# Kernel tuning notes

Measured on AMD Instinct MI355X. Metric: run time of the kernel, lower is better.

Reference implementation:

```python
import jax, jax.numpy as jnp
import numpy as np

CODEBOOK_SIZE = 1024
EMB_DIM = 256
BETA = 0.25


def setup_inputs() -> dict:
    key = jax.random.key(0)
    k1, k2 = jax.random.split(key)
    z = jax.random.normal(k1, (8, EMB_DIM, 16, 16, 16), dtype=jnp.float32)
    # torch init: uniform(-1/K, 1/K)
    emb = jax.random.uniform(k2, (CODEBOOK_SIZE, EMB_DIM), dtype=jnp.float32,
                             minval=-1.0 / CODEBOOK_SIZE, maxval=1.0 / CODEBOOK_SIZE)
    return {"z": z, "emb": emb}


def reference(z, emb):
    b, c, h, w, dd = z.shape
    K = emb.shape[0]
    # (b c h w d) -> (b h w d, c)
    zf = jnp.transpose(z, (0, 2, 3, 4, 1)).reshape(-1, c)  # [N, C]
    d = ((zf ** 2).sum(axis=1, keepdims=True)
         + (emb ** 2).sum(axis=1)
         - 2.0 * zf @ emb.T)  # [N, K]
    mean_distance = jnp.mean(d)
    idx = jnp.argmin(d, axis=1)  # [N]
    # one-hot @ codebook == gather
    zq = jnp.take(emb, idx, axis=0)  # [N, C]
    zq = jnp.transpose(zq.reshape(b, h, w, dd, c), (0, 4, 1, 2, 3))  # [b,c,h,w,d]
    loss = (jnp.mean((jax.lax.stop_gradient(zq) - z) ** 2)
            + BETA * jnp.mean((zq - jax.lax.stop_gradient(z)) ** 2))
    # straight-through estimator
    zq_st = z + jax.lax.stop_gradient(zq - z)
    # perplexity from code usage histogram (== mean of one-hot encodings)
    counts = jnp.zeros((K,), dtype=z.dtype).at[idx].add(1.0)
    e_mean = counts / idx.shape[0]
    perplexity = jnp.exp(-jnp.sum(e_mean * jnp.log(e_mean + 1e-10)))
    return zq_st, loss, perplexity, idx, mean_distance
```

## Files before the change

kernel.cpp:

```cpp
#include <hip/hip_runtime.h>
#include <math.h>

#define C 256
#define K 1024
#define SS 4096
#define NB 8
#define NN 32768
#define ZQ_ELEMS 8388608
#define OUT_LOSS 8388608
#define OUT_PERP 8388609
#define OUT_IDX  8388610
#define OUT_MD   8421378

#define WS_SZ2   0
#define WS_SE2   1
#define WS_LOSS  2
#define WS_ZSUM  8
#define WS_ESUM  264
#define WS_CNT   520
#define WS_E2R   1544
#define WS_Z2N   2568
#define WS_FLG   35336
#define WS_EH    68608
#define WS_CAND  330752

#define TC_FACT 1.8e-6f
#define TF_FACT 1.6e-6f
#define CAP 4
#define CAP_BIG 24
#define OV 7

typedef __attribute__((ext_vector_type(8))) short short8;
typedef __attribute__((ext_vector_type(4))) float f32x4;
typedef unsigned short u16;

__device__ inline u16 f2bf(float x) {
  unsigned u = __float_as_uint(x);
  unsigned r = (u + 0x7fffu + ((u >> 16) & 1u)) >> 16;
  return (u16)r;
}
__device__ inline float bf2f(u16 h) { return __uint_as_float(((unsigned)h) << 16); }

__device__ __forceinline__ void gl_lds16(const u16* g, u16* l) {
  __builtin_amdgcn_global_load_lds(
      (const __attribute__((address_space(1))) unsigned int*)g,
      (__attribute__((address_space(3))) unsigned int*)l,
      16, 0, 0);
}

__device__ inline float np_sumsq_256(const float* __restrict__ a) {
  float tot = 0.f;
  #pragma unroll
  for (int h = 0; h < 2; ++h) {
    const float* p = a + 128 * h;
    float r[8];
    #pragma unroll
    for (int j = 0; j < 8; ++j) r[j] = __fmul_rn(p[j], p[j]);
    for (int i = 8; i < 128; i += 8) {
      #pragma unroll
      for (int j = 0; j < 8; ++j) {
        float v = p[i + j];
        r[j] = __fadd_rn(r[j], __fmul_rn(v, v));
      }
    }
    float s01 = __fadd_rn(r[0], r[1]);
    float s23 = __fadd_rn(r[2], r[3]);
    float s45 = __fadd_rn(r[4], r[5]);
    float s67 = __fadd_rn(r[6], r[7]);
    float res = __fadd_rn(__fadd_rn(s01, s23), __fadd_rn(s45, s67));
    tot = (h == 0) ? res : __fadd_rn(tot, res);
  }
  return tot;
}

__global__ __launch_bounds__(256)
void emb_prep_k(const float* __restrict__ emb, float* __restrict__ ws,
                u16* __restrict__ eh) {
  int r0 = blockIdx.x * 16;
  int t = threadIdx.x;
  float s = 0.f;
  #pragma unroll
  for (int i = 0; i < 16; ++i) {
    size_t idx = (size_t)(r0 + i) * C + t;
    float v = emb[idx];
    s += v;
    eh[idx] = f2bf(v);
  }
  atomicAdd(&ws[WS_ESUM + t], s);
  if (t < 16) {
    float e2 = np_sumsq_256(emb + (size_t)(r0 + t) * C);
    ws[WS_E2R + r0 + t] = e2;
    atomicAdd(&ws[WS_SE2], e2);
  }
}

#define MROWS 64
#define ZS_STRIDE 260

__global__ __launch_bounds__(256)
void prep_z_k(const float* __restrict__ z, float* __restrict__ ws,
              u16* __restrict__ zh_g) {
  __shared__ float zs[MROWS * ZS_STRIDE];
  const int t = threadIdx.x;
  const int n0 = blockIdx.x * MROWS;
  const int b = n0 / SS;
  const int s0 = n0 % SS;
  {
    const int sl = t & 63, cg = t >> 6;
    const float* zb = z + (size_t)b * C * SS + s0 + sl;
    #pragma unroll
    for (int i = 0; i < 16; ++i) {
      int c = (cg * 16 + i) * 4;
      float4 v;
      v.x = zb[(size_t)(c + 0) * SS];
      v.y = zb[(size_t)(c + 1) * SS];
      v.z = zb[(size_t)(c + 2) * SS];
      v.w = zb[(size_t)(c + 3) * SS];
      *(float4*)&zs[sl * ZS_STRIDE + c] = v;
    }
  }
  __syncthreads();
  {
    float s = 0.f;
    #pragma unroll 8
    for (int r = 0; r < MROWS; ++r) s += zs[r * ZS_STRIDE + t];
    atomicAdd(&ws[WS_ZSUM + t], s);
  }
  {
    #pragma unroll
    for (int i = 0; i < 8; ++i) {
      int q = i * 256 + t;
      int row = q >> 5;
      int c0 = (q & 31) * 8;
      float4 va = *(const float4*)&zs[row * ZS_STRIDE + c0];
      float4 vb = *(const float4*)&zs[row * ZS_STRIDE + c0 + 4];
      float f[8] = {va.x, va.y, va.z, va.w, vb.x, vb.y, vb.z, vb.w};
      short8 hv;
      #pragma unroll
      for (int j = 0; j < 8; ++j) hv[j] = (short)f2bf(f[j]);
      *(short8*)&zh_g[(size_t)(n0 + row) * C + c0] = hv;
    }
  }
  if (t < MROWS) {
    float z2 = np_sumsq_256(&zs[t * ZS_STRIDE]);
    ws[WS_Z2N + n0 + t] = z2;
    #pragma unroll
    for (int off = 32; off; off >>= 1) z2 += __shfl_down(z2, off);
    if (t == 0) atomicAdd(&ws[WS_SZ2], z2);
  }
}

#define BM 64
#define BN 128
#define CH 64

__global__ __launch_bounds__(256, 2)
void vq_mfma_k(const u16* __restrict__ zh_g, const u16* __restrict__ eh_g,
               const float* __restrict__ e2row, const float* __restrict__ z2np,
               float* __restrict__ out_idx,
               int* __restrict__ qarr, u16* __restrict__ cand) {
  extern __shared__ u16 smem_u16[];
  u16* Ah2 = smem_u16;
  u16* Bh2 = Ah2 + 2 * BM * CH;
  float* e2s = (float*)(Bh2 + 2 * BN * CH);
  float* z2s = e2s + BN;
  float* lval = z2s + BM;
  unsigned* Mlds = (unsigned*)(lval + BM * CAP_BIG);
  unsigned* cntl = Mlds + BM;
  u16* lidx = (u16*)(cntl + BM);

  const int t = threadIdx.x;
  const int lane = t & 63;
  const int wid = t >> 6;
  const int wm = wid >> 1, wn = wid & 1;
  const int quad = lane >> 4, lr = lane & 15;
  const int row0 = blockIdx.x * BM;
  const int wrow = lane >> 3;
  const int pl = wrow * C + ((lane & 7) ^ wrow) * 8;

  if (t < BM) {
    z2s[t] = z2np[row0 + t];
    Mlds[t] = 0x7F800000u;
    cntl[t] = 0u;
  }

  {
    #pragma unroll
    for (int i = 0; i < 2; ++i) {
      int grow = (wid * 2 + i) * 8;
      gl_lds16(&zh_g[(size_t)(row0 + grow) * C + pl], &Ah2[grow * CH]);
    }
    #pragma unroll
    for (int i = 0; i < 4; ++i) {
      int grow = (wid * 4 + i) * 8;
      gl_lds16(&eh_g[(size_t)grow * C + pl], &Bh2[grow * CH]);
    }
  }
  __syncthreads();

  float v1[8], i1f[8];
  #pragma unroll
  for (int s = 0; s < 8; ++s) { v1[s] = 3.4e38f; i1f[s] = 0.f; }

  f32x4 acc[2][4];
  #pragma unroll
  for (int mi = 0; mi < 2; ++mi)
    #pragma unroll
    for (int ni = 0; ni < 4; ++ni) acc[mi][ni] = (f32x4){0.f, 0.f, 0.f, 0.f};

  int p = 0;
  for (int it = 0; it < 32; ++it) {
    const int nt = it >> 2, ch = it & 3;
    if (ch == 0 && t < BN) e2s[t] = e2row[nt * BN + t];
    if (it < 31) {
      const int ntn = (it + 1) >> 2, chn = (it + 1) & 3;
      const int c0n = chn * CH;
      u16* Ab = Ah2 + (p ^ 1) * (BM * CH);
      u16* Bb = Bh2 + (p ^ 1) * (BN * CH);
      #pragma unroll
      for (int i = 0; i < 2; ++i) {
        int grow = (wid * 2 + i) * 8;
        gl_lds16(&zh_g[(size_t)(row0 + grow) * C + c0n + pl], &Ab[grow * CH]);
      }
      #pragma unroll
      for (int i = 0; i < 4; ++i) {
        int grow = (wid * 4 + i) * 8;
        gl_lds16(&eh_g[(size_t)(ntn * BN + grow) * C + c0n + pl], &Bb[grow * CH]);
      }
    }
    {
      const u16* Ab = Ah2 + p * (BM * CH);
      const u16* Bb = Bh2 + p * (BN * CH);
      #pragma unroll
      for (int s = 0; s < 2; ++s) {
        const int q = s * 4 + quad;
        short8 af[2];
        #pragma unroll
        for (int mi = 0; mi < 2; ++mi) {
          int rowl = wm * 32 + mi * 16 + lr;
          int jp = q ^ (rowl & 7);
          af[mi] = *(const short8*)&Ab[rowl * CH + jp * 8];
        }
        #pragma unroll
        for (int ni = 0; ni < 4; ++ni) {
          int rowb = wn * 64 + ni * 16 + lr;
          int jp = q ^ (rowb & 7);
          short8 bh = *(const short8*)&Bb[rowb * CH + jp * 8];
          #pragma unroll
          for (int mi = 0; mi < 2; ++mi)
            acc[mi][ni] = __builtin_amdgcn_mfma_f32_16x16x32_bf16(af[mi], bh, acc[mi][ni], 0, 0, 0);
        }
      }
    }
    if (ch == 3) {
      const int kc0 = nt * BN;
      #pragma unroll
      for (int mi = 0; mi < 2; ++mi)
        #pragma unroll
        for (int r = 0; r < 4; ++r) {
          const int slot = mi * 4 + r;
          const int row = wm * 32 + mi * 16 + quad * 4 + r;
          const float z2r = z2s[row];
          float dqv[4];
          #pragma unroll
          for (int ni = 0; ni < 4; ++ni)
            dqv[ni] = __fsub_rn(__fadd_rn(z2r, e2s[wn * 64 + ni * 16 + lr]),
                                __fmul_rn(2.f, acc[mi][ni][r]));
          float mm = fminf(fminf(dqv[0], dqv[1]), fminf(dqv[2], dqv[3]));
          #pragma unroll
          for (int off = 1; off < 16; off <<= 1)
            mm = fminf(mm, __shfl_xor(mm, off));
          if (lr == 0) atomicMin(&Mlds[row], __float_as_uint(mm));
          float Mst = __uint_as_float(Mlds[row]);
          float base = fminf(mm, Mst);
          float thr = fmaf(base, TC_FACT, base);
          #pragma unroll
          for (int ni = 0; ni < 4; ++ni) {
            float dq = dqv[ni];
            int col = kc0 + wn * 64 + ni * 16 + lr;
            if (dq < v1[slot]) { v1[slot] = dq; i1f[slot] = (float)col; }
            if (dq < thr) {
              unsigned pp = atomicAdd(&cntl[row], 1u);
              if (pp < CAP_BIG) {
                lval[row * CAP_BIG + pp] = dq;
                lidx[row * CAP_BIG + pp] = (u16)col;
              }
            }
            acc[mi][ni][r] = 0.f;
          }
        }
    }
    __syncthreads();
    p ^= 1;
  }

  #pragma unroll
  for (int off = 1; off < 16; off <<= 1) {
    #pragma unroll
    for (int s = 0; s < 8; ++s) {
      float ov1 = __shfl_xor(v1[s], off);
      float oi1 = __shfl_xor(i1f[s], off);
      bool take = (ov1 < v1[s]) || (ov1 == v1[s] && oi1 < i1f[s]);
      if (take) { v1[s] = ov1; i1f[s] = oi1; }
    }
  }
  __syncthreads();
  float* mv1 = (float*)Ah2;
  float* mi1 = mv1 + 2 * BM;
  if (lr == 0) {
    #pragma unroll
    for (int mi = 0; mi < 2; ++mi)
      #pragma unroll
      for (int r = 0; r < 4; ++r) {
        int slot = mi * 4 + r;
        int row = wm * 32 + mi * 16 + quad * 4 + r;
        mv1[wn * BM + row] = v1[slot];
        mi1[wn * BM + row] = i1f[slot];
      }
  }
  __syncthreads();
  if (t < BM) {
    float a1 = mv1[t], ai = mi1[t];
    float c1 = mv1[BM + t], ci = mi1[BM + t];
    bool take = (c1 < a1) || (c1 == a1 && ci < ai);
    float b1 = take ? c1 : a1;
    float bi = take ? ci : ai;
    out_idx[row0 + t] = bi;
    unsigned raw = cntl[t];
    float tf = fmaf(b1, TF_FACT, b1);
    int c = 0;
    u16 keep[CAP];
    bool ovf = raw > (unsigned)CAP_BIG;
    if (!ovf) {
      for (unsigned j = 0; j < raw; ++j) {
        if (lval[t * CAP_BIG + j] <= tf) {
          if (c < CAP) keep[c] = lidx[t * CAP_BIG + j];
          ++c;
        }
      }
      if (c > CAP) ovf = true;
    }
    if (ovf) {
      int o = atomicAdd(&qarr[1], 1);
      qarr[2 + NN - 1 - o] = row0 + t;
    } else if (c > 1) {
      int q = atomicAdd(&qarr[0], 1);
      qarr[2 + q] = (row0 + t) | (c << 16);
      #pragma unroll
      for (int j = 0; j < CAP; ++j)
        cand[(size_t)q * CAP + j] = (j < c) ? keep[j] : (u16)0;
    }
  }
}

__global__ __launch_bounds__(256)
void fixup_k(const float* __restrict__ z, const float* __restrict__ emb,
             const float* __restrict__ e2np, const float* __restrict__ z2np,
             const int* __restrict__ qarr, const u16* __restrict__ cand,
             float* __restrict__ out_idx) {
  int qcnt = qarr[0];
  if (qcnt > NN) qcnt = NN;
  const int t = threadIdx.x;
  const int lane = t & 63, w = t >> 6;
  for (int q = blockIdx.x * 4 + w; q < qcnt; q += gridDim.x * 4) {
    int e = qarr[2 + q];
    int n = e & 0xffff;
    int c = e >> 16;
    int b = n >> 12, s = n & (SS - 1);
    float z2 = z2np[n];
    const float* zb = z + (((size_t)b * C) << 12) + s;
    float4 zv;
    zv.x = zb[((size_t)(lane * 4 + 0)) << 12];
    zv.y = zb[((size_t)(lane * 4 + 1)) << 12];
    zv.z = zb[((size_t)(lane * 4 + 2)) << 12];
    zv.w = zb[((size_t)(lane * 4 + 3)) << 12];
    float bestd = 3.4e38f;
    int besti = 0x7fffffff;
    for (int j = 0; j < c; ++j) {
      int kk = (int)cand[(size_t)q * CAP + j];
      const float4 ev = *(const float4*)&emb[(size_t)kk * C + lane * 4];
      double acc = (double)zv.x * (double)ev.x;
      acc = fma((double)zv.y, (double)ev.y, acc);
      acc = fma((double)zv.z, (double)ev.z, acc);
      acc = fma((double)zv.w, (double)ev.w, acc);
      #pragma unroll
      for (int off = 32; off; off >>= 1) acc += __shfl_xor(acc, off);
      float g  = (float)acc;
      float t1 = __fadd_rn(z2, e2np[kk]);
      float d  = __fsub_rn(t1, __fmul_rn(2.f, g));
      if (d < bestd || (d == bestd && kk < besti)) { bestd = d; besti = kk; }
    }
    if (lane == 0) out_idx[n] = (float)besti;
  }
}

__global__ __launch_bounds__(256)
void fixov_k(const float* __restrict__ z, const float* __restrict__ emb,
             const float* __restrict__ e2np, const float* __restrict__ z2np,
             const int* __restrict__ qarr, float* __restrict__ out_idx) {
  __shared__ float zrow[C];
  __shared__ float bv[4];
  __shared__ int   bx[4];
  int novr = qarr[1];
  if (novr > NN) novr = NN;
  const int t = threadIdx.x;
  const int lane = t & 63, w = t >> 6;
  for (int o = blockIdx.x; o < novr; o += gridDim.x) {
    int n = qarr[2 + NN - 1 - o];
    int b = n >> 12, s = n & (SS - 1);
    __syncthreads();
    zrow[t] = z[((size_t)(b * C + t) << 12) + s];
    __syncthreads();
    float z2 = z2np[n];
    float best = 3.4e38f; int besti = 0x7fffffff;
    for (int kk = t; kk < K; kk += 256) {
      const float* er = emb + (size_t)kk * C;
      double a0 = 0.0, a1 = 0.0, a2 = 0.0, a3 = 0.0;
      for (int c = 0; c < C; c += 4) {
        a0 = fma((double)zrow[c + 0], (double)er[c + 0], a0);
        a1 = fma((double)zrow[c + 1], (double)er[c + 1], a1);
        a2 = fma((double)zrow[c + 2], (double)er[c + 2], a2);
        a3 = fma((double)zrow[c + 3], (double)er[c + 3], a3);
      }
      float g = (float)((a0 + a1) + (a2 + a3));
      float t1 = __fadd_rn(z2, e2np[kk]);
      float d  = __fsub_rn(t1, __fmul_rn(2.f, g));
      if (d < best || (d == best && kk < besti)) { best = d; besti = kk; }
    }
    #pragma unroll
    for (int off = 32; off; off >>= 1) {
      float ov = __shfl_down(best, off);
      int   oi = __shfl_down(besti, off);
      if (ov < best || (ov == best && oi < besti)) { best = ov; besti = oi; }
    }
    if (lane == 0) { bv[w] = best; bx[w] = besti; }
    __syncthreads();
    if (t == 0) {
      #pragma unroll
      for (int w2 = 1; w2 < 4; ++w2)
        if (bv[w2] < best || (bv[w2] == best && bx[w2] < besti)) {
          best = bv[w2]; besti = bx[w2];
        }
      out_idx[n] = (float)besti;
    }
  }
}

#define GROWS 64
__global__ __launch_bounds__(256)
void gather2_k(const float* __restrict__ z, const float* __restrict__ emb,
               float* __restrict__ out, float* __restrict__ ws,
               float* __restrict__ counts) {
  __shared__ float eb[GROWS * 257];
  __shared__ int idxs[GROWS];
  __shared__ float sc[4];
  const int t = threadIdx.x;
  const int n0 = blockIdx.x * GROWS;
  const int b = n0 >> 12;
  const int s0 = n0 & (SS - 1);
  if (t < GROWS) {
    int id = (int)out[OUT_IDX + n0 + t];
    idxs[t] = id;
    atomicAdd(&counts[id], 1.0f);
  }
  __syncthreads();
  #pragma unroll
  for (int i = 0; i < 16; ++i) {
    int q = i * 256 + t;
    int row = q >> 6, c4 = q & 63;
    float4 v = *(const float4*)&emb[(size_t)idxs[row] * C + c4 * 4];
    int base = row * 257 + c4 * 4;
    eb[base + 0] = v.x; eb[base + 1] = v.y;
    eb[base + 2] = v.z; eb[base + 3] = v.w;
  }
  __syncthreads();
  const int sl = t & 63, cg = t >> 6;
  const float* zb = z + (size_t)b * C * SS + s0 + sl;
  float* ob = out + (size_t)b * C * SS + s0 + sl;
  float l = 0.f;
  #pragma unroll 4
  for (int i = 0; i < 64; ++i) {
    int c = cg * 64 + i;
    float q = eb[sl * 257 + c];
    float zv = zb[(size_t)c * SS];
    float d = q - zv;
    l += d * d;
    ob[(size_t)c * SS] = q;
  }
  #pragma unroll
  for (int off = 32; off; off >>= 1) l += __shfl_down(l, off);
  int lane = t & 63, w = t >> 6;
  if (lane == 0) sc[w] = l;
  __syncthreads();
  if (t == 0)
    atomicAdd(&ws[WS_LOSS], sc[0] + sc[1] + sc[2] + sc[3]);
}

__global__ void finalize_k(const float* __restrict__ ws, float* __restrict__ out) {
  __shared__ float sc[8];
  int t = threadIdx.x;
  float ent = 0.f;
  #pragma unroll
  for (int k = t; k < K; k += 256) {
    float em = ws[WS_CNT + k] * (1.0f / NN);
    ent += em * logf(em + 1e-10f);
  }
  float zd = ws[WS_ZSUM + t] * ws[WS_ESUM + t];
  #pragma unroll
  for (int off = 32; off; off >>= 1) {
    ent += __shfl_down(ent, off);
    zd  += __shfl_down(zd, off);
  }
  int lane = t & 63, w = t >> 6;
  if (lane == 0) { sc[w] = ent; sc[4 + w] = zd; }
  __syncthreads();
  if (t == 0) {
    ent = sc[0] + sc[1] + sc[2] + sc[3];
    zd  = sc[4] + sc[5] + sc[6] + sc[7];
    out[OUT_LOSS] = 1.25f * ws[WS_LOSS] * (1.0f / ZQ_ELEMS);
    out[OUT_PERP] = expf(-ent);
    out[OUT_MD]   = ws[WS_SZ2] * (1.0f / NN) + ws[WS_SE2] * (1.0f / K)
                  - 2.0f * zd * (1.0f / ((float)NN * (float)K));
  }
}

extern "C" void kernel_launch(void* const* d_in, const int* in_sizes, int n_in,
                              void* d_out, int out_size, void* d_ws, size_t ws_size,
                              hipStream_t stream) {
  const float* z   = (const float*)d_in[0];
  const float* emb = (const float*)d_in[1];
  float* out = (float*)d_out;
  float* ws  = (float*)d_ws;
  int* qarr = (int*)(ws + WS_FLG);
  u16* cand = (u16*)(ws + WS_CAND);
  u16* eh_g = (u16*)(ws + WS_EH);
  u16* zh_g = (u16*)d_out;
  (void)in_sizes; (void)n_in; (void)out_size; (void)ws_size;

  hipMemsetAsync(d_ws, 0, WS_E2R * sizeof(float), stream);
  hipMemsetAsync(ws + WS_FLG, 0, 2 * sizeof(int), stream);
  emb_prep_k<<<64, 256, 0, stream>>>(emb, ws, eh_g);
  prep_z_k<<<NN / MROWS, 256, 0, stream>>>(z, ws, zh_g);
  size_t lds = (size_t)(2 * BM * CH + 2 * BN * CH) * sizeof(u16)
             + (size_t)(BN + BM + BM * CAP_BIG) * sizeof(float)
             + (size_t)(2 * BM) * sizeof(unsigned)
             + (size_t)(BM * CAP_BIG) * sizeof(u16);
  vq_mfma_k<<<NN / BM, 256, lds, stream>>>(zh_g, eh_g,
                                           ws + WS_E2R, ws + WS_Z2N,
                                           out + OUT_IDX, qarr, cand);
  fixup_k<<<2048, 256, 0, stream>>>(z, emb, ws + WS_E2R, ws + WS_Z2N,
                                    qarr, cand, out + OUT_IDX);
  fixov_k<<<512, 256, 0, stream>>>(z, emb, ws + WS_E2R, ws + WS_Z2N,
                                   qarr, out + OUT_IDX);
  gather2_k<<<NN / GROWS, 256, 0, stream>>>(z, emb, out, ws, ws + WS_CNT);
  finalize_k<<<1, 256, 0, stream>>>(ws, out);
}
```

Baseline: 241.1 us.

## Keep z tile in registers and deepen codebook LDS pipeline to four stages

The distance GEMM kernel now loads each block's full 64x256 bf16 z tile straight into registers once, instead of streaming it through LDS every iteration. The codebook tiles go through a 4-slot LDS ring, prefetched two steps ahead and guarded by explicit s_waitcnt/s_barrier in place of a full __syncthreads each step. All 1024 codebook norms are also staged into LDS once up front. This removes repeated A-tile LDS traffic and barrier stalls, at the cost of many more VGPRs (areg holds 16 short8 per lane) and hand-tuned waitcnt counts that must match the outstanding loads exactly.

```diff
diff --git a/kernel.cpp b/kernel.cpp
--- a/kernel.cpp
+++ b/kernel.cpp
@@ -160,10 +160,9 @@
                float* __restrict__ out_idx,
                int* __restrict__ qarr, u16* __restrict__ cand) {
   extern __shared__ u16 smem_u16[];
-  u16* Ah2 = smem_u16;
-  u16* Bh2 = Ah2 + 2 * BM * CH;
-  float* e2s = (float*)(Bh2 + 2 * BN * CH);
-  float* z2s = e2s + BN;
+  u16* Bh4 = smem_u16;
+  float* e2all = (float*)(Bh4 + 4 * BN * CH);
+  float* z2s  = e2all + K;
   float* lval = z2s + BM;
   unsigned* Mlds = (unsigned*)(lval + BM * CAP_BIG);
   unsigned* cntl = Mlds + BM;
@@ -178,120 +177,114 @@
   const int wrow = lane >> 3;
   const int pl = wrow * C + ((lane & 7) ^ wrow) * 8;
 
+  #pragma unroll
+  for (int i = 0; i < 4; ++i) e2all[i * 256 + t] = e2row[i * 256 + t];
   if (t < BM) {
     z2s[t] = z2np[row0 + t];
     Mlds[t] = 0x7F800000u;
     cntl[t] = 0u;
   }
-
-  {
-    #pragma unroll
-    for (int i = 0; i < 2; ++i) {
-      int grow = (wid * 2 + i) * 8;
-      gl_lds16(&zh_g[(size_t)(row0 + grow) * C + pl], &Ah2[grow * CH]);
-    }
+  short8 areg[4][2][2];
+  #pragma unroll
+  for (int ch = 0; ch < 4; ++ch)
+    #pragma unroll
+    for (int s = 0; s < 2; ++s)
+      #pragma unroll
+      for (int mi = 0; mi < 2; ++mi)
+        areg[ch][s][mi] = *(const short8*)
+          &zh_g[(size_t)(row0 + wm * 32 + mi * 16 + lr) * C + ch * CH + (s * 4 + quad) * 8];
+
+  auto stageB = [&](int j) {
+    u16* Bb = Bh4 + (j & 3) * (BN * CH);
+    const u16* srcb = eh_g + (size_t)(j >> 2) * (BN * C) + (j & 3) * CH;
     #pragma unroll
     for (int i = 0; i < 4; ++i) {
       int grow = (wid * 4 + i) * 8;
-      gl_lds16(&eh_g[(size_t)grow * C + pl], &Bh2[grow * CH]);
-    }
-  }
+      gl_lds16(&srcb[(size_t)grow * C + pl], &Bb[grow * CH]);
+    }
+  };
+  stageB(0);
+  stageB(1);
   __syncthreads();
 
   float v1[8], i1f[8];
   #pragma unroll
   for (int s = 0; s < 8; ++s) { v1[s] = 3.4e38f; i1f[s] = 0.f; }
-
   f32x4 acc[2][4];
   #pragma unroll
   for (int mi = 0; mi < 2; ++mi)
     #pragma unroll
     for (int ni = 0; ni < 4; ++ni) acc[mi][ni] = (f32x4){0.f, 0.f, 0.f, 0.f};
 
-  int p = 0;
-  for (int it = 0; it < 32; ++it) {
-    const int nt = it >> 2, ch = it & 3;
-    if (ch == 0 && t < BN) e2s[t] = e2row[nt * BN + t];
-    if (it < 31) {
-      const int ntn = (it + 1) >> 2, chn = (it + 1) & 3;
-      const int c0n = chn * CH;
-      u16* Ab = Ah2 + (p ^ 1) * (BM * CH);
-      u16* Bb = Bh2 + (p ^ 1) * (BN * CH);
-      #pragma unroll
-      for (int i = 0; i < 2; ++i) {
-        int grow = (wid * 2 + i) * 8;
-        gl_lds16(&zh_g[(size_t)(row0 + grow) * C + c0n + pl], &Ab[grow * CH]);
-      }
-      #pragma unroll
-      for (int i = 0; i < 4; ++i) {
-        int grow = (wid * 4 + i) * 8;
-        gl_lds16(&eh_g[(size_t)(ntn * BN + grow) * C + c0n + pl], &Bb[grow * CH]);
-      }
-    }
-    {
-      const u16* Ab = Ah2 + p * (BM * CH);
-      const u16* Bb = Bh2 + p * (BN * CH);
+  for (int nt = 0; nt < 8; ++nt) {
+    #pragma unroll
+    for (int ch = 0; ch < 4; ++ch) {
+      const int it = nt * 4 + ch;
+      if (ch < 2) stageB(it + 2);
+      else if (nt < 7) stageB(it + 2);
+      if (ch < 2) {
+        asm volatile("s_waitcnt vmcnt(8) lgkmcnt(0)" ::: "memory");
+      } else if (ch == 2) {
+        if (nt < 7) asm volatile("s_waitcnt vmcnt(8) lgkmcnt(0)" ::: "memory");
+        else        asm volatile("s_waitcnt vmcnt(4) lgkmcnt(0)" ::: "memory");
+      } else {
+        if (nt < 7) asm volatile("s_waitcnt vmcnt(8) lgkmcnt(0)" ::: "memory");
+        else        asm volatile("s_waitcnt vmcnt(0) lgkmcnt(0)" ::: "memory");
+      }
+      __builtin_amdgcn_s_barrier();
+      const u16* Bb = Bh4 + ch * (BN * CH);
       #pragma unroll
       for (int s = 0; s < 2; ++s) {
-        const int q = s * 4 + quad;
-        short8 af[2];
-        #pragma unroll
-        for (int mi = 0; mi < 2; ++mi) {
-          int rowl = wm * 32 + mi * 16 + lr;
-          int jp = q ^ (rowl & 7);
-          af[mi] = *(const short8*)&Ab[rowl * CH + jp * 8];
-        }
         #pragma unroll
         for (int ni = 0; ni < 4; ++ni) {
           int rowb = wn * 64 + ni * 16 + lr;
-          int jp = q ^ (rowb & 7);
+          int jp = (s * 4 + quad) ^ (rowb & 7);
           short8 bh = *(const short8*)&Bb[rowb * CH + jp * 8];
           #pragma unroll
           for (int mi = 0; mi < 2; ++mi)
-            acc[mi][ni] = __builtin_amdgcn_mfma_f32_16x16x32_bf16(af[mi], bh, acc[mi][ni], 0, 0, 0);
+            acc[mi][ni] = __builtin_amdgcn_mfma_f32_16x16x32_bf16(
+                areg[ch][s][mi], bh, acc[mi][ni], 0, 0, 0);
         }
       }
-    }
-    if (ch == 3) {
-      const int kc0 = nt * BN;
-      #pragma unroll
-      for (int mi = 0; mi < 2; ++mi)
+      if (ch == 3) {
+        const int kc0 = nt * BN;
         #pragma unroll
-        for (int r = 0; r < 4; ++r) {
-          const int slot = mi * 4 + r;
-          const int row = wm * 32 + mi * 16 + quad * 4 + r;
-          const float z2r = z2s[row];
-          float dqv[4];
+        for (int mi = 0; mi < 2; ++mi)
           #pragma unroll
-          for (int ni = 0; ni < 4; ++ni)
-            dqv[ni] = __fsub_rn(__fadd_rn(z2r, e2s[wn * 64 + ni * 16 + lr]),
-                                __fmul_rn(2.f, acc[mi][ni][r]));
-          float mm = fminf(fminf(dqv[0], dqv[1]), fminf(dqv[2], dqv[3]));
-          #pragma unroll
-          for (int off = 1; off < 16; off <<= 1)
-            mm = fminf(mm, __shfl_xor(mm, off));
-          if (lr == 0) atomicMin(&Mlds[row], __float_as_uint(mm));
-          float Mst = __uint_as_float(Mlds[row]);
-          float base = fminf(mm, Mst);
-          float thr = fmaf(base, TC_FACT, base);
-          #pragma unroll
-          for (int ni = 0; ni < 4; ++ni) {
-            float dq = dqv[ni];
-            int col = kc0 + wn * 64 + ni * 16 + lr;
-            if (dq < v1[slot]) { v1[slot] = dq; i1f[slot] = (float)col; }
-            if (dq < thr) {
-              unsigned pp = atomicAdd(&cntl[row], 1u);
-              if (pp < CAP_BIG) {
-                lval[row * CAP_BIG + pp] = dq;
-                lidx[row * CAP_BIG + pp] = (u16)col;
+          for (int r = 0; r < 4; ++r) {
+            const int slot = mi * 4 + r;
+            const int row = wm * 32 + mi * 16 + quad * 4 + r;
+            const float z2r = z2s[row];
+            float dqv[4];
+            #pragma unroll
+            for (int ni = 0; ni < 4; ++ni)
+              dqv[ni] = __fsub_rn(__fadd_rn(z2r, e2all[kc0 + wn * 64 + ni * 16 + lr]),
+                                  __fmul_rn(2.f, acc[mi][ni][r]));
+            float mm = fminf(fminf(dqv[0], dqv[1]), fminf(dqv[2], dqv[3]));
+            #pragma unroll
+            for (int off = 1; off < 16; off <<= 1)
+              mm = fminf(mm, __shfl_xor(mm, off));
+            if (lr == 0) atomicMin(&Mlds[row], __float_as_uint(mm));
+            float Mst = __uint_as_float(Mlds[row]);
+            float base = fminf(mm, Mst);
+            float thr = fmaf(base, TC_FACT, base);
+            #pragma unroll
+            for (int ni = 0; ni < 4; ++ni) {
+              float dq = dqv[ni];
+              int col = kc0 + wn * 64 + ni * 16 + lr;
+              if (dq < v1[slot]) { v1[slot] = dq; i1f[slot] = (float)col; }
+              if (dq < thr) {
+                unsigned pp = atomicAdd(&cntl[row], 1u);
+                if (pp < CAP_BIG) {
+                  lval[row * CAP_BIG + pp] = dq;
+                  lidx[row * CAP_BIG + pp] = (u16)col;
+                }
               }
+              acc[mi][ni][r] = 0.f;
             }
-            acc[mi][ni][r] = 0.f;
           }
-        }
-    }
-    __syncthreads();
-    p ^= 1;
+      }
+    }
   }
 
   #pragma unroll
@@ -305,7 +298,7 @@
     }
   }
   __syncthreads();
-  float* mv1 = (float*)Ah2;
+  float* mv1 = (float*)Bh4;
   float* mi1 = mv1 + 2 * BM;
   if (lr == 0) {
     #pragma unroll
@@ -541,8 +534,8 @@
   hipMemsetAsync(ws + WS_FLG, 0, 2 * sizeof(int), stream);
   emb_prep_k<<<64, 256, 0, stream>>>(emb, ws, eh_g);
   prep_z_k<<<NN / MROWS, 256, 0, stream>>>(z, ws, zh_g);
-  size_t lds = (size_t)(2 * BM * CH + 2 * BN * CH) * sizeof(u16)
-             + (size_t)(BN + BM + BM * CAP_BIG) * sizeof(float)
+  size_t lds = (size_t)(4 * BN * CH) * sizeof(u16)
+             + (size_t)(K + BM + BM * CAP_BIG) * sizeof(float)
              + (size_t)(2 * BM) * sizeof(unsigned)
              + (size_t)(BM * CAP_BIG) * sizeof(u16);
   vq_mfma_k<<<NN / BM, 256, lds, stream>>>(zh_g, eh_g,
```

Result: faster. 233.5 us (-3.1%).
